# Kernel tuning notes

Measured on AMD Instinct MI355X. Metric: run time of the kernel, lower is better.

The kernel has to match this reference:

```python
import jax, jax.numpy as jnp
import numpy as np

D = 512; N = 4096; NH = 16; DEPTH = 3; MLP = 4; GENES = 250; GH = 64; GW = 64


def setup_inputs() -> dict:
    key = jax.random.key(0)
    ks = jax.random.split(key, 10)
    gf = jax.random.normal(ks[0], (N, D), jnp.float32)
    # unique spot positions: permutation of the 64x64 grid cells
    perm = jax.random.permutation(ks[1], GH * GW)[:N]
    coords = jnp.stack([perm // GW, perm % GW], axis=1).astype(jnp.int32)
    s = 0.02
    rn = lambda k, sh: jax.random.normal(k, sh, jnp.float32) * s
    return dict(
        global_feats=gf, coords=coords, grid_h=GH, grid_w=GW,
        ln1_g=jnp.ones((DEPTH, D)), ln1_b=jnp.zeros((DEPTH, D)),
        wqkv=rn(ks[2], (DEPTH, 3 * D, D)), bqkv=jnp.zeros((DEPTH, 3 * D)),
        wo=rn(ks[3], (DEPTH, D, D)), bo=jnp.zeros((DEPTH, D)),
        ln2_g=jnp.ones((DEPTH, D)), ln2_b=jnp.zeros((DEPTH, D)),
        w1=rn(ks[4], (DEPTH, MLP * D, D)), b1=jnp.zeros((DEPTH, MLP * D)),
        w2=rn(ks[5], (DEPTH, D, MLP * D)), b2=jnp.zeros((DEPTH, D)),
        ck=rn(ks[6], (DEPTH, D, 1, 3, 3)), cb=jnp.zeros((DEPTH, D)),
        lnf_g=jnp.ones((D,)), lnf_b=jnp.zeros((D,)),
        wp=rn(ks[7], (GENES, D)), bp=jnp.zeros((GENES,)),
    )


def _ln(x, g, b, eps=1e-5):
    m = jnp.mean(x, axis=-1, keepdims=True)
    v = jnp.var(x, axis=-1, keepdims=True)
    return (x - m) * jax.lax.rsqrt(v + eps) * g + b


def reference(global_feats, coords, grid_h, grid_w, ln1_g, ln1_b, wqkv, bqkv,
              wo, bo, ln2_g, ln2_b, w1, b1, w2, b2, ck, cb, lnf_g, lnf_b, wp, bp):
    x = global_feats  # [N, D]
    n, d = x.shape
    nh = NH; dh = d // nh
    rows = coords[:, 0]; cols = coords[:, 1]
    for i in range(ln1_g.shape[0]):
        # --- self-attention (eval mode, dropout off) ---
        xn = _ln(x, ln1_g[i], ln1_b[i])
        qkv = xn @ wqkv[i].T + bqkv[i]                      # [N, 3D]
        q, k, v = jnp.split(qkv, 3, axis=-1)
        q = q.reshape(n, nh, dh).transpose(1, 0, 2)        # [H, N, dh]
        k = k.reshape(n, nh, dh).transpose(1, 0, 2)
        v = v.reshape(n, nh, dh).transpose(1, 0, 2)
        att = jax.nn.softmax(jnp.einsum('hqd,hkd->hqk', q, k) * (dh ** -0.5), axis=-1)
        ao = jnp.einsum('hqk,hkd->hqd', att, v).transpose(1, 0, 2).reshape(n, d)
        x = x + (ao @ wo[i].T + bo[i])
        # --- MLP ---
        h = jax.nn.gelu(_ln(x, ln2_g[i], ln2_b[i]) @ w1[i].T + b1[i], approximate=False)
        x = x + (h @ w2[i].T + b2[i])
        # --- APEG: scatter -> depthwise conv -> gather ---
        grid = jnp.zeros((d, grid_h, grid_w), x.dtype).at[:, rows, cols].set(x.T)
        co = jax.lax.conv_general_dilated(
            grid[None], ck[i], window_strides=(1, 1), padding=((1, 1), (1, 1)),
            dimension_numbers=('NCHW', 'OIHW', 'NCHW'), feature_group_count=d)[0]
        co = co + cb[i][:, None, None]
        x = x + co[:, rows, cols].T
    x = _ln(x, lnf_g, lnf_b)
    pred = x @ wp.T + bp
    return (x, pred)
```

## Files before the change

kernel.cpp:

```cpp
#include <hip/hip_runtime.h>
#include <math.h>

#define D 512
#define N_TOK 4096
#define NHEAD 16
#define DH 32
#define DEPTH 3
#define MLPD 2048
#define GENES 250
#define GH 64
#define GW 64

typedef __attribute__((ext_vector_type(8))) short short8;
typedef __attribute__((ext_vector_type(4))) float f32x4;
typedef unsigned short ushort_t;

#define AS1 __attribute__((address_space(1)))
#define AS3 __attribute__((address_space(3)))

#if defined(__has_builtin)
#if __has_builtin(__builtin_amdgcn_exp2f)
#define EXP2F(x) __builtin_amdgcn_exp2f(x)
#endif
#endif
#ifndef EXP2F
#define EXP2F(x) __expf(0.69314718056f * (x))
#endif

__device__ __forceinline__ unsigned short f2bf(float f) {
  unsigned int u = __float_as_uint(f);
  u += 0x7fffu + ((u >> 16) & 1u);
  return (unsigned short)(u >> 16);
}
__device__ __forceinline__ unsigned int bfpack(float a, float b) {
  return __builtin_amdgcn_perm(__float_as_uint(b), __float_as_uint(a), 0x07060302u);
}
__device__ __forceinline__ void gload_lds16(const ushort_t* g, ushort_t* l) {
  __builtin_amdgcn_global_load_lds(
      (const AS1 unsigned int*)g,
      (AS3 unsigned int*)(unsigned int)(unsigned long long)l, 16, 0, 0);
}
__device__ __forceinline__ int perm64(int m) {
  int mi = m >> 4, g = (m >> 2) & 3, r = m & 3;
  return ((mi & 1) << 5) | (g << 3) | ((mi >> 1) << 2) | r;
}

__global__ __launch_bounds__(256) void ln_kernel(const float* __restrict__ x,
    const float* __restrict__ g, const float* __restrict__ b,
    float* __restrict__ yf, ushort_t* __restrict__ ybf) {
  int row = blockIdx.x;
  int t = threadIdx.x;
  const float* xr = x + (size_t)row * D;
  float v0 = xr[t], v1 = xr[t + 256];
  float s = v0 + v1;
  float sq = v0 * v0 + v1 * v1;
#pragma unroll
  for (int off = 32; off > 0; off >>= 1) {
    s += __shfl_down(s, off, 64);
    sq += __shfl_down(sq, off, 64);
  }
  __shared__ float s1[4], s2[4];
  int wid = t >> 6, lane = t & 63;
  if (lane == 0) { s1[wid] = s; s2[wid] = sq; }
  __syncthreads();
  float tot = s1[0] + s1[1] + s1[2] + s1[3];
  float totq = s2[0] + s2[1] + s2[2] + s2[3];
  float mean = tot * (1.0f / D);
  float var = totq * (1.0f / D) - mean * mean;
  float rs = rsqrtf(var + 1e-5f);
  float r0 = (v0 - mean) * rs * g[t] + b[t];
  float r1 = (v1 - mean) * rs * g[t + 256] + b[t + 256];
  if (yf) { yf[(size_t)row * D + t] = r0; yf[(size_t)row * D + t + 256] = r1; }
  if (ybf) {
    ybf[(size_t)row * D + t] = f2bf(r0);
    ybf[(size_t)row * D + t + 256] = f2bf(r1);
  }
}

template <int TM, int TN, int NKH>
__global__ __launch_bounds__(256) void gemm_bf(
    const ushort_t* __restrict__ A, const ushort_t* __restrict__ B,
    const float* __restrict__ bias, const float* __restrict__ res,
    float* __restrict__ C, ushort_t* __restrict__ Cbf,
    ushort_t* __restrict__ qO, ushort_t* __restrict__ kO, ushort_t* __restrict__ vO,
    int K, int ldc, int nstore, int mode) {
  constexpr int MI = TM / 32;
  constexpr int NI = TN / 32;
  __shared__ ushort_t As[2][NKH][TM * 32];
  __shared__ ushort_t Bs[2][NKH][TN * 32];
  int t = threadIdx.x;
  int w = t >> 6, lane = t & 63;
  int g = lane >> 4, c = lane & 15;
  int bm = blockIdx.y * TM, bn = blockIdx.x * TN;
  int wr = (w >> 1) * (TM / 2);
  int wc = (w & 1) * (TN / 2);

  const ushort_t* gA = A + (size_t)(bm + (t >> 2)) * K + (t & 3) * 8;
  const ushort_t* gB = B + (size_t)(bn + (t >> 2)) * K + (t & 3) * 8;

  auto stage = [&](int p, int koff) {
#pragma unroll
    for (int h = 0; h < NKH; ++h) {
      gload_lds16(gA + koff + h * 32, &As[p][h][t * 8]);
      if (TM == 128)
        gload_lds16(gA + koff + h * 32 + (size_t)64 * K, &As[p][h][(t + 256) * 8]);
      gload_lds16(gB + koff + h * 32, &Bs[p][h][t * 8]);
      if (TN == 128)
        gload_lds16(gB + koff + h * 32 + (size_t)64 * K, &Bs[p][h][(t + 256) * 8]);
    }
  };

  f32x4 acc[MI][NI] = {};

  const int niter = K / (32 * NKH);
  stage(0, 0);
  __syncthreads();
  for (int it = 0; it < niter; ++it) {
    int p = it & 1;
    if (it + 1 < niter) stage(p ^ 1, (it + 1) * 32 * NKH);
#pragma unroll
    for (int kh = 0; kh < NKH; ++kh) {
      short8 af[MI], bfr[NI];
#pragma unroll
      for (int mi = 0; mi < MI; ++mi)
        af[mi] = *(const short8*)&As[p][kh][(wr + mi * 16 + c) * 32 + g * 8];
#pragma unroll
      for (int ni = 0; ni < NI; ++ni)
        bfr[ni] = *(const short8*)&Bs[p][kh][(wc + ni * 16 + c) * 32 + g * 8];
#pragma unroll
      for (int mi = 0; mi < MI; ++mi)
#pragma unroll
        for (int ni = 0; ni < NI; ++ni)
          acc[mi][ni] = __builtin_amdgcn_mfma_f32_16x16x32_bf16(
              af[mi], bfr[ni], acc[mi][ni], 0, 0, 0);
    }
    __syncthreads();
  }

  const float qs_scale = 0.17677669529663688f * 1.4426950408889634f;
  if (mode == 2) {
#pragma unroll
    for (int ni = 0; ni < NI; ++ni) {
      int col = bn + wc + ni * 16 + c;
      float bv = bias[col];
      int which = col >> 9;
      int h = (col >> 5) & 15;
      int d = col & 31;
      size_t hb = (size_t)h * (N_TOK * DH);
#pragma unroll
      for (int mi = 0; mi < MI; ++mi) {
        int row0 = bm + wr + mi * 16 + g * 4;
        float v0 = acc[mi][ni][0] + bv;
        float v1 = acc[mi][ni][1] + bv;
        float v2 = acc[mi][ni][2] + bv;
        float v3 = acc[mi][ni][3] + bv;
        if (which == 0) {
          qO[hb + (size_t)(row0 + 0) * DH + d] = f2bf(v0 * qs_scale);
          qO[hb + (size_t)(row0 + 1) * DH + d] = f2bf(v1 * qs_scale);
          qO[hb + (size_t)(row0 + 2) * DH + d] = f2bf(v2 * qs_scale);
          qO[hb + (size_t)(row0 + 3) * DH + d] = f2bf(v3 * qs_scale);
        } else if (which == 1) {
          kO[hb + (size_t)(row0 + 0) * DH + d] = f2bf(v0);
          kO[hb + (size_t)(row0 + 1) * DH + d] = f2bf(v1);
          kO[hb + (size_t)(row0 + 2) * DH + d] = f2bf(v2);
          kO[hb + (size_t)(row0 + 3) * DH + d] = f2bf(v3);
        } else {
          int m = row0 & 63;
          int mi_l = m >> 4, g_l = (m >> 2) & 3;
          int nb = ((mi_l & 1) << 5) | (g_l << 3) | ((mi_l >> 1) << 2);
          uint2 pk;
          pk.x = (unsigned)f2bf(v0) | ((unsigned)f2bf(v1) << 16);
          pk.y = (unsigned)f2bf(v2) | ((unsigned)f2bf(v3) << 16);
          *(uint2*)(vO + hb + (size_t)d * N_TOK + (row0 & ~63) + nb) = pk;
        }
      }
    }
    return;
  }
#pragma unroll
  for (int ni = 0; ni < NI; ++ni) {
    int col = bn + wc + ni * 16 + c;
    float bv = bias[col];
    bool cok = col < nstore;
#pragma unroll
    for (int mi = 0; mi < MI; ++mi) {
      int row0 = bm + wr + mi * 16 + g * 4;
#pragma unroll
      for (int reg = 0; reg < 4; ++reg) {
        int row = row0 + reg;
        float v = acc[mi][ni][reg] + bv;
        if (mode == 0) {
          size_t idx = (size_t)row * ldc + col;
          if (cok) {
            if (res) v += res[idx];
            C[idx] = v;
          }
        } else {
          v = 0.5f * v * (1.0f + erff(v * 0.70710678118654752f));
          Cbf[(size_t)row * ldc + col] = f2bf(v);
        }
      }
    }
  }
}

#define KST 40
#define VTST 72

__global__ __launch_bounds__(256) void attn_mfma(
    const ushort_t* __restrict__ qb, const ushort_t* __restrict__ kb,
    const ushort_t* __restrict__ vtb, ushort_t* __restrict__ ao) {
  __shared__ ushort_t Ks[64 * KST];
  __shared__ ushort_t Vts[32 * VTST];
  int qt = blockIdx.x, head = blockIdx.y;
  int t = threadIdx.x;
  int w = t >> 6, lane = t & 63;
  int g = lane >> 4, c = lane & 15;
  const size_t hbase = (size_t)head * (N_TOK * DH);
  int q0 = qt * 128 + w * 32;

  short8 qf[2];
  qf[0] = *(const short8*)(qb + hbase + (size_t)(q0 + c) * DH + g * 8);
  qf[1] = *(const short8*)(qb + hbase + (size_t)(q0 + 16 + c) * DH + g * 8);

  short8 ones;
#pragma unroll
  for (int i = 0; i < 8; ++i) ones[i] = (short)0x3F80;

  f32x4 o[2][2] = {};
  f32x4 lf[2] = {};
  const f32x4 zf = {0.f, 0.f, 0.f, 0.f};

  const ushort_t* kg = kb + hbase + (size_t)(t >> 2) * DH + (t & 3) * 8;
  const ushort_t* vg = vtb + hbase + (size_t)(t >> 3) * N_TOK + (t & 7) * 8;
  ushort_t* kw = &Ks[(t >> 2) * KST + (t & 3) * 8];
  ushort_t* vw = &Vts[(t >> 3) * VTST + (t & 7) * 8];

  short8 kreg = *(const short8*)kg;
  short8 vreg = *(const short8*)vg;

  typedef union { short8 s8; unsigned int u32[4]; } pk_t;

  for (int tile = 0; tile < N_TOK / 64; ++tile) {
    __syncthreads();
    *(short8*)kw = kreg;
    *(short8*)vw = vreg;
    __syncthreads();
    if (tile + 1 < N_TOK / 64) {
      kreg = *(const short8*)(kg + (size_t)(tile + 1) * 64 * DH);
      vreg = *(const short8*)(vg + (tile + 1) * 64);
    }

    short8 kf[4];
#pragma unroll
    for (int mi = 0; mi < 4; ++mi)
      kf[mi] = *(const short8*)&Ks[(mi * 16 + c) * KST + g * 8];
    short8 vf[2][2];
#pragma unroll
    for (int half = 0; half < 2; ++half)
#pragma unroll
      for (int ch = 0; ch < 2; ++ch)
        vf[half][ch] = *(const short8*)&Vts[(half * 16 + c) * VTST + ch * 32 + g * 8];

    short8 pf[2][2];
#pragma unroll
    for (int qs = 0; qs < 2; ++qs) {
      f32x4 sp[4];
#pragma unroll
      for (int mi = 0; mi < 4; ++mi)
        sp[mi] = __builtin_amdgcn_mfma_f32_16x16x32_bf16(kf[mi], qf[qs], zf, 0, 0, 0);
      float pr[4][4];
#pragma unroll
      for (int mi = 0; mi < 4; ++mi)
#pragma unroll
        for (int r = 0; r < 4; ++r) pr[mi][r] = EXP2F(sp[mi][r]);
      pk_t p0, p1;
      p0.u32[0] = bfpack(pr[0][0], pr[0][1]);
      p0.u32[1] = bfpack(pr[0][2], pr[0][3]);
      p0.u32[2] = bfpack(pr[2][0], pr[2][1]);
      p0.u32[3] = bfpack(pr[2][2], pr[2][3]);
      p1.u32[0] = bfpack(pr[1][0], pr[1][1]);
      p1.u32[1] = bfpack(pr[1][2], pr[1][3]);
      p1.u32[2] = bfpack(pr[3][0], pr[3][1]);
      p1.u32[3] = bfpack(pr[3][2], pr[3][3]);
      pf[qs][0] = p0.s8;
      pf[qs][1] = p1.s8;
    }

#pragma unroll
    for (int qs = 0; qs < 2; ++qs) {
#pragma unroll
      for (int ch = 0; ch < 2; ++ch) {
        lf[qs] = __builtin_amdgcn_mfma_f32_16x16x32_bf16(ones, pf[qs][ch], lf[qs], 0, 0, 0);
#pragma unroll
        for (int half = 0; half < 2; ++half)
          o[qs][half] = __builtin_amdgcn_mfma_f32_16x16x32_bf16(
              vf[half][ch], pf[qs][ch], o[qs][half], 0, 0, 0);
      }
    }
  }

#pragma unroll
  for (int qs = 0; qs < 2; ++qs) {
    float inv = 1.0f / lf[qs][0];
    int q = q0 + qs * 16 + c;
    ushort_t* op = ao + (size_t)q * D + head * DH;
#pragma unroll
    for (int half = 0; half < 2; ++half)
#pragma unroll
      for (int reg = 0; reg < 4; ++reg)
        op[half * 16 + g * 4 + reg] = f2bf(o[qs][half][reg] * inv);
  }
}

__global__ void scatter_kernel(const int* __restrict__ coords,
                               int* __restrict__ pos2tok) {
  int n = blockIdx.x * 256 + threadIdx.x;
  if (n < N_TOK) pos2tok[coords[2 * n] * GW + coords[2 * n + 1]] = n;
}

__global__ __launch_bounds__(256) void conv_ln_kernel(
    const float* __restrict__ xin, float* __restrict__ xout,
    const float* __restrict__ ck, const float* __restrict__ cb,
    const int* __restrict__ pos2tok, const int* __restrict__ coords,
    const float* __restrict__ g, const float* __restrict__ b,
    float* __restrict__ yf, ushort_t* __restrict__ ybf) {
  int n = blockIdx.x, t = threadIdx.x;
  __shared__ int nb[9];
  if (t < 9) {
    int r = coords[2 * n], c = coords[2 * n + 1];
    int dy = t / 3 - 1, dx = t % 3 - 1;
    int rr = r + dy, cc = c + dx;
    nb[t] = (rr >= 0 && rr < GH && cc >= 0 && cc < GW) ? pos2tok[rr * GW + cc] : -1;
  }
  __syncthreads();
  float v[2];
#pragma unroll
  for (int j = 0; j < 2; ++j) {
    int ch = t + j * 256;
    float s = cb[ch];
#pragma unroll
    for (int tap = 0; tap < 9; ++tap) {
      int tok = nb[tap];
      if (tok >= 0) s = fmaf(ck[ch * 9 + tap], xin[(size_t)tok * D + ch], s);
    }
    v[j] = xin[(size_t)n * D + ch] + s;
    xout[(size_t)n * D + ch] = v[j];
  }
  float s = v[0] + v[1];
  float sq = v[0] * v[0] + v[1] * v[1];
#pragma unroll
  for (int off = 32; off > 0; off >>= 1) {
    s += __shfl_down(s, off, 64);
    sq += __shfl_down(sq, off, 64);
  }
  __shared__ float s1[4], s2[4];
  int wid = t >> 6, lane = t & 63;
  if (lane == 0) { s1[wid] = s; s2[wid] = sq; }
  __syncthreads();
  float tot = s1[0] + s1[1] + s1[2] + s1[3];
  float totq = s2[0] + s2[1] + s2[2] + s2[3];
  float mean = tot * (1.0f / D);
  float var = totq * (1.0f / D) - mean * mean;
  float rs = rsqrtf(var + 1e-5f);
  float r0 = (v[0] - mean) * rs * g[t] + b[t];
  float r1 = (v[1] - mean) * rs * g[t + 256] + b[t + 256];
  if (yf) { yf[(size_t)n * D + t] = r0; yf[(size_t)n * D + t + 256] = r1; }
  ybf[(size_t)n * D + t] = f2bf(r0);
  ybf[(size_t)n * D + t + 256] = f2bf(r1);
}

__global__ __launch_bounds__(256) void castw(const float* __restrict__ src,
    ushort_t* __restrict__ dst, int n_src, int n_dst) {
  int i = (blockIdx.x * 256 + threadIdx.x) * 4;
  if (i >= n_dst) return;
  unsigned long long pk = 0;
#pragma unroll
  for (int j = 0; j < 4; ++j) {
    float v = (i + j < n_src) ? src[i + j] : 0.f;
    pk |= ((unsigned long long)f2bf(v)) << (16 * j);
  }
  *(unsigned long long*)(dst + i) = pk;
}

__global__ void pad_bias(const float* __restrict__ src, float* __restrict__ dst) {
  int i = threadIdx.x;
  dst[i] = (i < GENES) ? src[i] : 0.f;
}

extern "C" void kernel_launch(void* const* d_in, const int* in_sizes, int n_in,
                              void* d_out, int out_size, void* d_ws, size_t ws_size,
                              hipStream_t stream) {
  const float* gf     = (const float*)d_in[0];
  const int*   coords = (const int*)d_in[1];
  const float* ln1_g  = (const float*)d_in[4];
  const float* ln1_b  = (const float*)d_in[5];
  const float* wqkv   = (const float*)d_in[6];
  const float* bqkv   = (const float*)d_in[7];
  const float* wo     = (const float*)d_in[8];
  const float* bo     = (const float*)d_in[9];
  const float* ln2_g  = (const float*)d_in[10];
  const float* ln2_b  = (const float*)d_in[11];
  const float* w1     = (const float*)d_in[12];
  const float* b1     = (const float*)d_in[13];
  const float* w2     = (const float*)d_in[14];
  const float* b2     = (const float*)d_in[15];
  const float* ck     = (const float*)d_in[16];
  const float* cb     = (const float*)d_in[17];
  const float* lnf_g  = (const float*)d_in[18];
  const float* lnf_b  = (const float*)d_in[19];
  const float* wp     = (const float*)d_in[20];
  const float* bp     = (const float*)d_in[21];
  float* out = (float*)d_out;

  const size_t ND = (size_t)N_TOK * D;
  float* xb0 = (float*)d_ws;
  float* xb1 = xb0 + ND;
  ushort_t* xn_bf  = (ushort_t*)(xb1 + ND);
  ushort_t* ao_bf  = xn_bf + ND;
  ushort_t* out_bf = ao_bf + ND;
  ushort_t* shared = out_bf + ND;
  ushort_t* qb   = shared;
  ushort_t* kbuf = qb + ND;
  ushort_t* vtb  = kbuf + ND;
  ushort_t* h_bf = shared;
  ushort_t* wqkv_bf = shared + (size_t)N_TOK * MLPD;
  ushort_t* wo_bf = wqkv_bf + DEPTH * 3 * D * D;
  ushort_t* w1_bf = wo_bf + DEPTH * D * D;
  ushort_t* w2_bf = w1_bf + DEPTH * MLPD * D;
  ushort_t* wp_bf = w2_bf + DEPTH * D * MLPD;
  float* bp_pad = (float*)(wp_bf + 256 * D);
  int* pos2tok = (int*)(bp_pad + 256);

  hipMemcpyAsync(xb0, gf, ND * sizeof(float), hipMemcpyDeviceToDevice, stream);
  hipMemsetAsync(pos2tok, 0xFF, GH * GW * sizeof(int), stream);
  scatter_kernel<<<(N_TOK + 255) / 256, 256, 0, stream>>>(coords, pos2tok);

  int nw;
  nw = DEPTH * 3 * D * D;  castw<<<(nw / 4 + 255) / 256, 256, 0, stream>>>(wqkv, wqkv_bf, nw, nw);
  nw = DEPTH * D * D;      castw<<<(nw / 4 + 255) / 256, 256, 0, stream>>>(wo, wo_bf, nw, nw);
  nw = DEPTH * MLPD * D;   castw<<<(nw / 4 + 255) / 256, 256, 0, stream>>>(w1, w1_bf, nw, nw);
  nw = DEPTH * D * MLPD;   castw<<<(nw / 4 + 255) / 256, 256, 0, stream>>>(w2, w2_bf, nw, nw);
  castw<<<(256 * D / 4 + 255) / 256, 256, 0, stream>>>(wp, wp_bf, GENES * D, 256 * D);
  pad_bias<<<1, 256, 0, stream>>>(bp, bp_pad);

  ln_kernel<<<N_TOK, 256, 0, stream>>>(xb0, ln1_g, ln1_b, nullptr, xn_bf);

  float* x  = xb0;
  float* xo = xb1;
  for (int i = 0; i < DEPTH; ++i) {
    gemm_bf<128, 64, 1><<<dim3(24, 32), 256, 0, stream>>>(
        xn_bf, wqkv_bf + (size_t)i * 3 * D * D, bqkv + (size_t)i * 3 * D,
        nullptr, nullptr, nullptr, qb, kbuf, vtb, D, 0, 3 * D, 2);
    attn_mfma<<<dim3(N_TOK / 128, NHEAD), 256, 0, stream>>>(qb, kbuf, vtb, ao_bf);
    gemm_bf<64, 64, 2><<<dim3(8, 64), 256, 0, stream>>>(
        ao_bf, wo_bf + (size_t)i * D * D, bo + (size_t)i * D,
        x, x, nullptr, nullptr, nullptr, nullptr, D, D, D, 0);
    ln_kernel<<<N_TOK, 256, 0, stream>>>(x, ln2_g + i * D, ln2_b + i * D, nullptr, xn_bf);
    gemm_bf<128, 64, 1><<<dim3(32, 32), 256, 0, stream>>>(
        xn_bf, w1_bf + (size_t)i * MLPD * D, b1 + (size_t)i * MLPD,
        nullptr, nullptr, h_bf, nullptr, nullptr, nullptr, D, MLPD, MLPD, 1);
    gemm_bf<64, 64, 2><<<dim3(8, 64), 256, 0, stream>>>(
        h_bf, w2_bf + (size_t)i * D * MLPD, b2 + (size_t)i * D,
        x, x, nullptr, nullptr, nullptr, nullptr, MLPD, D, D, 0);
    if (i < DEPTH - 1) {
      conv_ln_kernel<<<N_TOK, 256, 0, stream>>>(
          x, xo, ck + (size_t)i * D * 9, cb + (size_t)i * D, pos2tok, coords,
          ln1_g + (i + 1) * D, ln1_b + (i + 1) * D, nullptr, xn_bf);
    } else {
      conv_ln_kernel<<<N_TOK, 256, 0, stream>>>(
          x, xo, ck + (size_t)i * D * 9, cb + (size_t)i * D, pos2tok, coords,
          lnf_g, lnf_b, out, out_bf);
    }
    float* tmp = x; x = xo; xo = tmp;
  }
  gemm_bf<64, 64, 2><<<dim3(4, 64), 256, 0, stream>>>(
      out_bf, wp_bf, bp_pad, nullptr, out + ND, nullptr, nullptr, nullptr, nullptr,
      D, GENES, GENES, 0);
}
```

Before: 621.6 us.

## Load K fragments directly from global and double-buffer V tile in attention

The attention kernel stops staging K through shared memory. Each lane loads its K MFMA fragments straight from global memory into a double-buffered register set, one tile ahead. V^T is double-buffered in shared memory, so each iteration needs one barrier instead of two. s_setprio is raised around the MFMA blocks so the matrix work gets scheduling priority over other waves. This trades more register pressure and redundant global K loads across the four waves for fewer LDS round-trips and barriers.

```diff
diff --git a/kernel.cpp b/kernel.cpp
--- a/kernel.cpp
+++ b/kernel.cpp
@@ -204,14 +204,12 @@
   }
 }
 
-#define KST 40
 #define VTST 72
 
 __global__ __launch_bounds__(256) void attn_mfma(
     const ushort_t* __restrict__ qb, const ushort_t* __restrict__ kb,
     const ushort_t* __restrict__ vtb, ushort_t* __restrict__ ao) {
-  __shared__ ushort_t Ks[64 * KST];
-  __shared__ ushort_t Vts[32 * VTST];
+  __shared__ ushort_t Vts[2][32 * VTST];
   int qt = blockIdx.x, head = blockIdx.y;
   int t = threadIdx.x;
   int w = t >> 6, lane = t & 63;
@@ -231,44 +229,52 @@
   f32x4 lf[2] = {};
   const f32x4 zf = {0.f, 0.f, 0.f, 0.f};
 
-  const ushort_t* kg = kb + hbase + (size_t)(t >> 2) * DH + (t & 3) * 8;
   const ushort_t* vg = vtb + hbase + (size_t)(t >> 3) * N_TOK + (t & 7) * 8;
-  ushort_t* kw = &Ks[(t >> 2) * KST + (t & 3) * 8];
-  ushort_t* vw = &Vts[(t >> 3) * VTST + (t & 7) * 8];
-
-  short8 kreg = *(const short8*)kg;
-  short8 vreg = *(const short8*)vg;
-
+  const int vofs = (t >> 3) * VTST + (t & 7) * 8;
+  const ushort_t* kp = kb + hbase + (size_t)c * DH + g * 8;
+
+  constexpr int NT = N_TOK / 64;
   typedef union { short8 s8; unsigned int u32[4]; } pk_t;
 
-  for (int tile = 0; tile < N_TOK / 64; ++tile) {
-    __syncthreads();
-    *(short8*)kw = kreg;
-    *(short8*)vw = vreg;
-    __syncthreads();
-    if (tile + 1 < N_TOK / 64) {
-      kreg = *(const short8*)(kg + (size_t)(tile + 1) * 64 * DH);
-      vreg = *(const short8*)(vg + (tile + 1) * 64);
-    }
-
-    short8 kf[4];
-#pragma unroll
-    for (int mi = 0; mi < 4; ++mi)
-      kf[mi] = *(const short8*)&Ks[(mi * 16 + c) * KST + g * 8];
+  short8 kfb[2][4];
+#pragma unroll
+  for (int mi = 0; mi < 4; ++mi)
+    kfb[0][mi] = *(const short8*)(kp + (size_t)(mi * 16) * DH);
+  {
+    short8 v0 = *(const short8*)vg;
+    *(short8*)&Vts[0][vofs] = v0;
+  }
+  short8 vreg = *(const short8*)(vg + 64);
+  __syncthreads();
+
+#pragma unroll 2
+  for (int tile = 0; tile < NT; ++tile) {
+    const int p = tile & 1;
+    if (tile + 1 < NT) {
+      *(short8*)&Vts[p ^ 1][vofs] = vreg;
+      if (tile + 2 < NT) vreg = *(const short8*)(vg + (size_t)(tile + 2) * 64);
+#pragma unroll
+      for (int mi = 0; mi < 4; ++mi)
+        kfb[p ^ 1][mi] =
+            *(const short8*)(kp + (size_t)((tile + 1) * 64 + mi * 16) * DH);
+    }
+
     short8 vf[2][2];
 #pragma unroll
     for (int half = 0; half < 2; ++half)
 #pragma unroll
       for (int ch = 0; ch < 2; ++ch)
-        vf[half][ch] = *(const short8*)&Vts[(half * 16 + c) * VTST + ch * 32 + g * 8];
+        vf[half][ch] = *(const short8*)&Vts[p][(half * 16 + c) * VTST + ch * 32 + g * 8];
 
     short8 pf[2][2];
 #pragma unroll
     for (int qs = 0; qs < 2; ++qs) {
       f32x4 sp[4];
+      __builtin_amdgcn_s_setprio(1);
 #pragma unroll
       for (int mi = 0; mi < 4; ++mi)
-        sp[mi] = __builtin_amdgcn_mfma_f32_16x16x32_bf16(kf[mi], qf[qs], zf, 0, 0, 0);
+        sp[mi] = __builtin_amdgcn_mfma_f32_16x16x32_bf16(kfb[p][mi], qf[qs], zf, 0, 0, 0);
+      __builtin_amdgcn_s_setprio(0);
       float pr[4][4];
 #pragma unroll
       for (int mi = 0; mi < 4; ++mi)
@@ -287,6 +293,7 @@
       pf[qs][1] = p1.s8;
     }
 
+    __builtin_amdgcn_s_setprio(1);
 #pragma unroll
     for (int qs = 0; qs < 2; ++qs) {
 #pragma unroll
@@ -298,6 +305,8 @@
               vf[half][ch], pf[qs][ch], o[qs][half], 0, 0, 0);
       }
     }
+    __builtin_amdgcn_s_setprio(0);
+    __syncthreads();
   }
 
 #pragma unroll
```

After: 641.9 us. +3.3%, slower.

## Load K/V fragments directly from global with register double-buffering in attention

Applied to the files above, without the earlier changes.

The attention kernel stops staging K and V tiles through shared memory with two barriers per tile. Each wave now loads its MFMA fragments straight from global/L2 into two register buffers, prefetching two tiles ahead. Each wave also handles 64 queries instead of 32, which halves the grid to 256 blocks and reuses each K/V fragment across four query slices. In exchange, every wave fetches the whole K/V stream itself with no sharing inside the block, register pressure rises, and the smaller grid may leave some of the chip's CUs underused.

```diff
diff --git a/kernel.cpp b/kernel.cpp
--- a/kernel.cpp
+++ b/kernel.cpp
@@ -204,76 +204,65 @@
   }
 }
 
-#define KST 40
-#define VTST 72
-
 __global__ __launch_bounds__(256) void attn_mfma(
     const ushort_t* __restrict__ qb, const ushort_t* __restrict__ kb,
     const ushort_t* __restrict__ vtb, ushort_t* __restrict__ ao) {
-  __shared__ ushort_t Ks[64 * KST];
-  __shared__ ushort_t Vts[32 * VTST];
-  int qt = blockIdx.x, head = blockIdx.y;
   int t = threadIdx.x;
   int w = t >> 6, lane = t & 63;
   int g = lane >> 4, c = lane & 15;
+  const int head = blockIdx.y;
   const size_t hbase = (size_t)head * (N_TOK * DH);
-  int q0 = qt * 128 + w * 32;
-
-  short8 qf[2];
-  qf[0] = *(const short8*)(qb + hbase + (size_t)(q0 + c) * DH + g * 8);
-  qf[1] = *(const short8*)(qb + hbase + (size_t)(q0 + 16 + c) * DH + g * 8);
+  int q0 = blockIdx.x * 256 + w * 64;
+
+  short8 qf[4];
+#pragma unroll
+  for (int qs = 0; qs < 4; ++qs)
+    qf[qs] = *(const short8*)(qb + hbase + (size_t)(q0 + qs * 16 + c) * DH + g * 8);
 
   short8 ones;
 #pragma unroll
   for (int i = 0; i < 8; ++i) ones[i] = (short)0x3F80;
 
-  f32x4 o[2][2] = {};
-  f32x4 lf[2] = {};
+  f32x4 o[4][2] = {};
+  f32x4 lf[4] = {};
   const f32x4 zf = {0.f, 0.f, 0.f, 0.f};
 
-  const ushort_t* kg = kb + hbase + (size_t)(t >> 2) * DH + (t & 3) * 8;
-  const ushort_t* vg = vtb + hbase + (size_t)(t >> 3) * N_TOK + (t & 7) * 8;
-  ushort_t* kw = &Ks[(t >> 2) * KST + (t & 3) * 8];
-  ushort_t* vw = &Vts[(t >> 3) * VTST + (t & 7) * 8];
-
-  short8 kreg = *(const short8*)kg;
-  short8 vreg = *(const short8*)vg;
-
+  const ushort_t* kp = kb + hbase + (size_t)c * DH + g * 8;
+  const ushort_t* vp = vtb + hbase + (size_t)c * N_TOK + g * 8;
+
+  constexpr int NT = N_TOK / 64;
   typedef union { short8 s8; unsigned int u32[4]; } pk_t;
 
-  for (int tile = 0; tile < N_TOK / 64; ++tile) {
-    __syncthreads();
-    *(short8*)kw = kreg;
-    *(short8*)vw = vreg;
-    __syncthreads();
-    if (tile + 1 < N_TOK / 64) {
-      kreg = *(const short8*)(kg + (size_t)(tile + 1) * 64 * DH);
-      vreg = *(const short8*)(vg + (tile + 1) * 64);
-    }
-
-    short8 kf[4];
+  auto loadK = [&](short8* kf, int tile) {
 #pragma unroll
     for (int mi = 0; mi < 4; ++mi)
-      kf[mi] = *(const short8*)&Ks[(mi * 16 + c) * KST + g * 8];
-    short8 vf[2][2];
+      kf[mi] = *(const short8*)(kp + (size_t)(tile * 64 + mi * 16) * DH);
+  };
+  auto loadV = [&](short8 (*vf)[2], int tile) {
 #pragma unroll
     for (int half = 0; half < 2; ++half)
 #pragma unroll
       for (int ch = 0; ch < 2; ++ch)
-        vf[half][ch] = *(const short8*)&Vts[(half * 16 + c) * VTST + ch * 32 + g * 8];
-
-    short8 pf[2][2];
-#pragma unroll
-    for (int qs = 0; qs < 2; ++qs) {
-      f32x4 sp[4];
+        vf[half][ch] =
+            *(const short8*)(vp + (size_t)(half * 16) * N_TOK + tile * 64 + ch * 32);
+  };
+
+  auto body = [&](short8* kf, short8 (*vf)[2], int tile) {
+    f32x4 sp[4][4];
+#pragma unroll
+    for (int qs = 0; qs < 4; ++qs)
 #pragma unroll
       for (int mi = 0; mi < 4; ++mi)
-        sp[mi] = __builtin_amdgcn_mfma_f32_16x16x32_bf16(kf[mi], qf[qs], zf, 0, 0, 0);
+        sp[qs][mi] = __builtin_amdgcn_mfma_f32_16x16x32_bf16(kf[mi], qf[qs], zf, 0, 0, 0);
+    if (tile + 2 < NT) loadK(kf, tile + 2);
+    short8 pf[4][2];
+#pragma unroll
+    for (int qs = 0; qs < 4; ++qs) {
       float pr[4][4];
 #pragma unroll
       for (int mi = 0; mi < 4; ++mi)
 #pragma unroll
-        for (int r = 0; r < 4; ++r) pr[mi][r] = EXP2F(sp[mi][r]);
+        for (int r = 0; r < 4; ++r) pr[mi][r] = EXP2F(sp[qs][mi][r]);
       pk_t p0, p1;
       p0.u32[0] = bfpack(pr[0][0], pr[0][1]);
       p0.u32[1] = bfpack(pr[0][2], pr[0][3]);
@@ -286,9 +275,8 @@
       pf[qs][0] = p0.s8;
       pf[qs][1] = p1.s8;
     }
-
-#pragma unroll
-    for (int qs = 0; qs < 2; ++qs) {
+#pragma unroll
+    for (int qs = 0; qs < 4; ++qs)
 #pragma unroll
       for (int ch = 0; ch < 2; ++ch) {
         lf[qs] = __builtin_amdgcn_mfma_f32_16x16x32_bf16(ones, pf[qs][ch], lf[qs], 0, 0, 0);
@@ -297,11 +285,23 @@
           o[qs][half] = __builtin_amdgcn_mfma_f32_16x16x32_bf16(
               vf[half][ch], pf[qs][ch], o[qs][half], 0, 0, 0);
       }
-    }
-  }
-
-#pragma unroll
-  for (int qs = 0; qs < 2; ++qs) {
+    if (tile + 2 < NT) loadV(vf, tile + 2);
+  };
+
+  short8 kA[4], kB[4];
+  short8 vA[2][2], vB[2][2];
+  loadK(kA, 0);
+  loadV(vA, 0);
+  loadK(kB, 1);
+  loadV(vB, 1);
+
+  for (int tile = 0; tile < NT; tile += 2) {
+    body(kA, vA, tile);
+    body(kB, vB, tile + 1);
+  }
+
+#pragma unroll
+  for (int qs = 0; qs < 4; ++qs) {
     float inv = 1.0f / lf[qs][0];
     int q = q0 + qs * 16 + c;
     ushort_t* op = ao + (size_t)q * D + head * DH;
@@ -452,7 +452,7 @@
     gemm_bf<128, 64, 1><<<dim3(24, 32), 256, 0, stream>>>(
         xn_bf, wqkv_bf + (size_t)i * 3 * D * D, bqkv + (size_t)i * 3 * D,
         nullptr, nullptr, nullptr, qb, kbuf, vtb, D, 0, 3 * D, 2);
-    attn_mfma<<<dim3(N_TOK / 128, NHEAD), 256, 0, stream>>>(qb, kbuf, vtb, ao_bf);
+    attn_mfma<<<dim3(N_TOK / 256, NHEAD), 256, 0, stream>>>(qb, kbuf, vtb, ao_bf);
     gemm_bf<64, 64, 2><<<dim3(8, 64), 256, 0, stream>>>(
         ao_bf, wo_bf + (size_t)i * D * D, bo + (size_t)i * D,
         x, x, nullptr, nullptr, nullptr, nullptr, D, D, D, 0);
```

Result: slower. 672.2 us (+8.1%).
